# Performance work log

Measured on AMD Instinct MI355X. Metric: run time of the kernel, lower is better.

The kernel has to match this reference:

```python
import jax, jax.numpy as jnp
import numpy as np

D_MODEL, D_HEAD, D_MLP, N_HEADS = 768, 64, 3072, 12
BATCH, SEQ = 1, 4096
LN_EPS = 1e-05
IGNORE = -100000.0


def setup_inputs() -> dict:
    key = jax.random.key(0)
    ks = jax.random.split(key, 8)
    s = 0.02
    return {
        "resid_pre": jax.random.normal(ks[0], (BATCH, SEQ, D_MODEL), jnp.float32),
        "ln1_w": jnp.ones((D_MODEL,), jnp.float32),
        "ln1_b": jnp.zeros((D_MODEL,), jnp.float32),
        "ln2_w": jnp.ones((D_MODEL,), jnp.float32),
        "ln2_b": jnp.zeros((D_MODEL,), jnp.float32),
        "W_Q": jax.random.normal(ks[1], (N_HEADS, D_MODEL, D_HEAD), jnp.float32) * s,
        "W_K": jax.random.normal(ks[2], (N_HEADS, D_MODEL, D_HEAD), jnp.float32) * s,
        "W_V": jax.random.normal(ks[3], (N_HEADS, D_MODEL, D_HEAD), jnp.float32) * s,
        "W_O": jax.random.normal(ks[4], (N_HEADS, D_HEAD, D_MODEL), jnp.float32) * s,
        "b_Q": jnp.zeros((N_HEADS, D_HEAD), jnp.float32),
        "b_K": jnp.zeros((N_HEADS, D_HEAD), jnp.float32),
        "b_V": jnp.zeros((N_HEADS, D_HEAD), jnp.float32),
        "b_O": jnp.zeros((D_MODEL,), jnp.float32),
        "W_in": jax.random.normal(ks[5], (D_MODEL, D_MLP), jnp.float32) * s,
        "b_in": jnp.zeros((D_MLP,), jnp.float32),
        "W_out": jax.random.normal(ks[6], (D_MLP, D_MODEL), jnp.float32) * s,
        "b_out": jnp.zeros((D_MODEL,), jnp.float32),
    }


def _layernorm(x, w, b):
    mean = jnp.mean(x, axis=-1, keepdims=True)
    var = jnp.var(x, axis=-1, keepdims=True)  # unbiased=False
    return (x - mean) * jax.lax.rsqrt(var + LN_EPS) * w + b


def _attention(x, W_Q, W_K, W_V, W_O, b_Q, b_K, b_V, b_O):
    # x: [b, s, d_model]; W_{Q,K,V}: [h, d_model, d_head]
    q = jnp.einsum("bsm,hmd->bshd", x, W_Q) + b_Q
    k = jnp.einsum("bsm,hmd->bshd", x, W_K) + b_K
    v = jnp.einsum("bsm,hmd->bshd", x, W_V) + b_V
    scores = jnp.einsum("bqhd,bkhd->bhqk", q, k) / np.sqrt(D_HEAD).astype(np.float32)
    seq = x.shape[1]
    causal = jnp.tril(jnp.ones((seq, seq), bool))  # True where allowed
    scores = jnp.where(causal, scores, IGNORE)
    pattern = jax.nn.softmax(scores, axis=-1)
    z = jnp.einsum("bkhd,bhqk->bqhd", v, pattern)
    return jnp.einsum("bqhd,hdm->bqm", z, W_O) + b_O


def reference(resid_pre, ln1_w, ln1_b, ln2_w, ln2_b,
              W_Q, W_K, W_V, W_O, b_Q, b_K, b_V, b_O,
              W_in, b_in, W_out, b_out):
    resid_mid = _attention(_layernorm(resid_pre, ln1_w, ln1_b),
                           W_Q, W_K, W_V, W_O, b_Q, b_K, b_V, b_O) + resid_pre
    pre = jnp.einsum("bsm,mf->bsf", _layernorm(resid_mid, ln2_w, ln2_b), W_in) + b_in
    post = jax.nn.gelu(pre, approximate=False)  # torch F.gelu default = exact erf
    mlp_out = jnp.einsum("bsf,fm->bsm", post, W_out) + b_out
    resid_post = mlp_out + resid_mid
    return (resid_post, post)
```

## Files before the change

kernel.cpp:

```cpp
#include <hip/hip_runtime.h>
#include <hip/hip_bf16.h>
#include <math.h>

using bf16 = __hip_bfloat16;
using u16  = unsigned short;
using u32  = unsigned int;
using short8 = __attribute__((ext_vector_type(8))) short;
using f32x4  = __attribute__((ext_vector_type(4))) float;

#define AS1 __attribute__((address_space(1)))
#define AS3 __attribute__((address_space(3)))

__device__ __forceinline__ void gld_lds16(const void* g, void* l) {
  __builtin_amdgcn_global_load_lds((const AS1 u32*)g, (AS3 u32*)l, 16, 0, 0);
}

__device__ __forceinline__ bool probe_f32(const void* p) {
  return *(const u32*)p == 0x3F800000u;
}
__device__ __forceinline__ float ldf(const void* p, size_t i, bool f32) {
  return f32 ? ((const float*)p)[i] : __bfloat162float(((const bf16*)p)[i]);
}
__device__ __forceinline__ void stf(void* p, size_t i, float v, bool f32) {
  if (f32) ((float*)p)[i] = v;
  else     ((bf16*)p)[i] = __float2bfloat16(v);
}
__device__ __forceinline__ u32 cvt_pk_bf16(float lo, float hi) {
  u32 r;
  asm("v_cvt_pk_bf16_f32 %0, %1, %2" : "=v"(r) : "v"(lo), "v"(hi));
  return r;
}

__global__ __launch_bounds__(256) void ln_kernel(const void* __restrict__ x,
    const void* __restrict__ w, const void* __restrict__ b, bf16* __restrict__ out,
    const void* probe, int x_is_f32)
{
  const bool pf = probe_f32(probe);
  const bool xf = x_is_f32 ? true : pf;
  const int row = blockIdx.x, t = threadIdx.x;
  const size_t base = (size_t)row * 768;
  float v[3]; float s1 = 0.f, s2 = 0.f;
#pragma unroll
  for (int i = 0; i < 3; ++i) { float f = ldf(x, base + i*256 + t, xf); v[i] = f; s1 += f; s2 += f*f; }
#pragma unroll
  for (int off = 32; off >= 1; off >>= 1) { s1 += __shfl_xor(s1, off); s2 += __shfl_xor(s2, off); }
  __shared__ float a1[4], a2[4];
  if ((t & 63) == 0) { a1[t>>6] = s1; a2[t>>6] = s2; }
  __syncthreads();
  float S1 = a1[0]+a1[1]+a1[2]+a1[3];
  float S2 = a2[0]+a2[1]+a2[2]+a2[3];
  float mean = S1 * (1.f/768.f);
  float var  = S2 * (1.f/768.f) - mean*mean;
  float rs = rsqrtf(var + 1e-5f);
#pragma unroll
  for (int i = 0; i < 3; ++i) {
    int c = i*256 + t;
    out[base + c] = __float2bfloat16((v[i]-mean)*rs*ldf(w, c, pf) + ldf(b, c, pf));
  }
}

__global__ __launch_bounds__(256) void prep_all(
    const void* W_Q, const void* W_K, const void* W_V, const void* Wo,
    const void* Win, const void* Wout,
    const void* bQ, const void* bK, const void* bV, const void* bO,
    const void* bIn, const void* bOut,
    bf16* __restrict__ qkvT, bf16* __restrict__ WoT, bf16* __restrict__ WinT,
    bf16* __restrict__ WoutT, float* __restrict__ biasA,
    const void* __restrict__ xres, const void* lw, const void* lb,
    bf16* __restrict__ lnout, const void* probe)
{
  const bool pf = probe_f32(probe);
  const int bid = blockIdx.x;
  const int t = threadIdx.x;
  if (bid >= 6939) {
    const int row = bid - 6939;
    const size_t base = (size_t)row * 768;
    float v[3]; float s1 = 0.f, s2 = 0.f;
#pragma unroll
    for (int i = 0; i < 3; ++i) { float f = ldf(xres, base + i*256 + t, pf); v[i] = f; s1 += f; s2 += f*f; }
#pragma unroll
    for (int off = 32; off >= 1; off >>= 1) { s1 += __shfl_xor(s1, off); s2 += __shfl_xor(s2, off); }
    __shared__ float a1[4], a2[4];
    if ((t & 63) == 0) { a1[t>>6] = s1; a2[t>>6] = s2; }
    __syncthreads();
    float S1 = a1[0]+a1[1]+a1[2]+a1[3];
    float S2 = a2[0]+a2[1]+a2[2]+a2[3];
    float mean = S1 * (1.f/768.f);
    float var  = S2 * (1.f/768.f) - mean*mean;
    float rs = rsqrtf(var + 1e-5f);
#pragma unroll
    for (int i = 0; i < 3; ++i) {
      int c = i*256 + t;
      lnout[base + c] = __float2bfloat16((v[i]-mean)*rs*ldf(lw, c, pf) + ldf(lb, c, pf));
    }
    return;
  }
  if (bid >= 6912) {
    int i = (bid - 6912)*256 + t;
    float v;
    if (i < 2304)      v = (i < 768) ? ldf(bQ, i, pf) : (i < 1536 ? ldf(bK, i-768, pf) : ldf(bV, i-1536, pf));
    else if (i < 3072) v = ldf(bO, i-2304, pf);
    else if (i < 6144) v = ldf(bIn, i-3072, pf);
    else               v = ldf(bOut, i-6144, pf);
    biasA[i] = v;
    return;
  }
  const void* src; bf16* dst; int R, C, bx, by; size_t soff = 0;
  if (bid < 1728) {
    int mtx = bid / 576, within = bid % 576;
    int h = within / 48, tt = within % 48;
    by = tt >> 1; bx = tt & 1;
    src = (mtx == 0) ? W_Q : (mtx == 1 ? W_K : W_V);
    soff = (size_t)h * 49152;
    dst = qkvT + ((size_t)mtx*768 + h*64) * 768;
    R = 768; C = 64;
  } else if (bid < 2304) {
    int within = bid - 1728; bx = within % 24; by = within / 24;
    src = Wo; dst = WoT; R = 768; C = 768;
  } else if (bid < 4608) {
    int within = bid - 2304; bx = within % 96; by = within / 96;
    src = Win; dst = WinT; R = 768; C = 3072;
  } else {
    int within = bid - 4608; bx = within % 24; by = within / 24;
    src = Wout; dst = WoutT; R = 3072; C = 768;
  }
  __shared__ bf16 tile[32][33];
  const int bc = bx*32, br = by*32;
  const int tx = t & 31, ty = t >> 5;
#pragma unroll
  for (int i = 0; i < 32; i += 8)
    tile[ty+i][tx] = __float2bfloat16(ldf(src, soff + (size_t)(br+ty+i)*C + bc + tx, pf));
  __syncthreads();
#pragma unroll
  for (int i = 0; i < 32; i += 8)
    dst[(size_t)(bc+ty+i)*R + br + tx] = tile[tx][ty+i];
}

template<int MODE, int BM, int BN, int BK>
__global__ __launch_bounds__(256) void gemm_bt(const bf16* __restrict__ A,
    const bf16* __restrict__ BT, const float* __restrict__ bias,
    const void* __restrict__ res, void* __restrict__ Cout, bf16* __restrict__ aux,
    size_t outOff, const void* probe, int M, int N, int K,
    float* __restrict__ zf, float* __restrict__ sf)
{
  constexpr int MR = BM/32, NR = BN/32;
  constexpr int CH = BK/8;
  __shared__ bf16 Alds[BM*BK];
  __shared__ bf16 Blds[BN*BK];
  const int tid = threadIdx.x;
  const int lane = tid & 63, w = tid >> 6;
  const int l15 = lane & 15, l4 = lane >> 4;

  if (MODE == 0) {
    int bid = blockIdx.y * gridDim.x + blockIdx.x;
    float4 z4 = {0.f, 0.f, 0.f, 0.f};
    float4* zp = (float4*)zf + (size_t)bid*1024;
#pragma unroll
    for (int i = 0; i < 4; ++i) zp[i*256 + tid] = z4;
    if (tid < 16) ((float4*)sf)[bid*16 + tid] = z4;
  }

  const int brow = blockIdx.y * BM, bcol = blockIdx.x * BN;
  const int wr = (w >> 1) * (BM/2), wc = (w & 1) * (BN/2);
  const bf16* Ag = A  + (size_t)brow * K;
  const bf16* Bg = BT + (size_t)bcol * K;
  f32x4 acc[MR][NR];
#pragma unroll
  for (int i = 0; i < MR; ++i)
#pragma unroll
    for (int j = 0; j < NR; ++j) acc[i][j] = 0.f;

  for (int kt = 0; kt < K; kt += BK) {
#pragma unroll
    for (int i = 0; i < BM*CH/256; ++i) {
      int id = i*256 + tid, r = id / CH, cc = id % CH;
      int sw = (r ^ (r >> 3)) & 7;
      gld_lds16(Ag + (size_t)r*K + kt + ((cc ^ sw) * 8), (char*)Alds + id*16);
    }
#pragma unroll
    for (int i = 0; i < BN*CH/256; ++i) {
      int id = i*256 + tid, r = id / CH, cc = id % CH;
      int sw = (r ^ (r >> 3)) & 7;
      gld_lds16(Bg + (size_t)r*K + kt + ((cc ^ sw) * 8), (char*)Blds + id*16);
    }
    __syncthreads();
#pragma unroll
    for (int kk = 0; kk < BK/32; ++kk) {
      short8 a[MR], b[NR];
#pragma unroll
      for (int mi = 0; mi < MR; ++mi) {
        int row = wr + mi*16 + l15, sw = (row ^ (row >> 3)) & 7;
        a[mi] = *(const short8*)((const char*)Alds + row*(BK*2) + (((kk*4 + l4) ^ sw) << 4));
      }
#pragma unroll
      for (int ni = 0; ni < NR; ++ni) {
        int row = wc + ni*16 + l15, sw = (row ^ (row >> 3)) & 7;
        b[ni] = *(const short8*)((const char*)Blds + row*(BK*2) + (((kk*4 + l4) ^ sw) << 4));
      }
      __builtin_amdgcn_s_setprio(1);
#pragma unroll
      for (int mi = 0; mi < MR; ++mi)
#pragma unroll
        for (int ni = 0; ni < NR; ++ni)
          acc[mi][ni] = __builtin_amdgcn_mfma_f32_16x16x32_bf16(a[mi], b[ni], acc[mi][ni], 0, 0, 0);
      __builtin_amdgcn_s_setprio(0);
    }
    __syncthreads();
  }

  const bool pf = probe_f32(probe);
#pragma unroll
  for (int mi = 0; mi < MR; ++mi) {
#pragma unroll
    for (int r = 0; r < 4; ++r) {
      int row = brow + wr + mi*16 + l4*4 + r;
      size_t rowoff = (size_t)row * N;
#pragma unroll
      for (int ni = 0; ni < NR; ++ni) {
        int col = bcol + wc + ni*16 + l15;
        float v = acc[mi][ni][r] + bias[col];
        if (MODE == 1) v += ldf(res, rowoff + col, pf);
        if (MODE == 3) v += ((const float*)res)[rowoff + col];
        if (MODE == 2) v = 0.5f * v * (1.0f + erff(v * 0.70710678118654752f));
        if (MODE == 0) ((bf16*)Cout)[rowoff + col] = __float2bfloat16(v);
        else if (MODE == 1) ((float*)Cout)[rowoff + col] = v;
        else {
          stf(Cout, outOff + rowoff + col, v, pf);
          if (MODE == 2) aux[rowoff + col] = __float2bfloat16(v);
        }
      }
    }
  }
}

__global__ __launch_bounds__(256) void attn_kernel(const bf16* __restrict__ QKV,
    float* __restrict__ Zf, float* __restrict__ Sf)
{
  __shared__ bf16 Ks[2][4096];
  __shared__ bf16 VTs[2][4096];
  __shared__ bf16 Ps[4][1024];
  const int cid = 159 - blockIdx.x, h = blockIdx.y;
  int qb, c;
  if (cid < 16)      { qb = cid;                    c = 0; }
  else if (cid < 48) { qb = 16 + ((cid-16) >> 1);   c = (cid-16) & 1; }
  else if (cid < 96) { qb = 32 + (cid-48)/3;        c = (cid-48)%3; }
  else               { qb = 48 + ((cid-96) >> 2);   c = (cid-96) & 3; }
  const int t_lo = c*16, t_hi = min(c*16 + 16, qb + 1);

  const int tid = threadIdx.x, lane = tid & 63, w = tid >> 6;
  const int l15 = lane & 15, l4 = lane >> 4;
  const int q0 = qb * 64;

  short8 qf[2];
#pragma unroll
  for (int kk = 0; kk < 2; ++kk)
    qf[kk] = *(const short8*)(QKV + (size_t)(q0 + w*16 + l15)*2304 + h*64 + kk*32 + l4*8);

  int kaddr[2][4], pst[4], pld[2], vwa[8];
#pragma unroll
  for (int kk = 0; kk < 2; ++kk)
#pragma unroll
    for (int ct = 0; ct < 4; ++ct) {
      int krow = ct*16 + l15, sk = (krow ^ (krow >> 3)) & 7;
      kaddr[kk][ct] = krow*128 + (((kk*4 + l4) ^ sk) << 4);
    }
#pragma unroll
  for (int r = 0; r < 4; ++r) {
    int prow = l4*4 + r, sp = (prow ^ (prow >> 3)) & 7;
    pst[r] = prow*128 + (((l15 >> 1) ^ sp) << 4) + (l15 & 1)*8;
  }
#pragma unroll
  for (int kg = 0; kg < 2; ++kg) {
    int sp2 = (l15 ^ (l15 >> 3)) & 7;
    pld[kg] = l15*128 + (((kg*4 + l4) ^ sp2) << 4);
  }
  const int vw = tid >> 3, vd0 = (tid & 7) * 8;
  const int vk0 = (vw >> 1) + (vw & 1) * 32;
#pragma unroll
  for (int d = 0; d < 8; ++d) {
    int row = vd0 + d, srow = (row ^ (row >> 3)) & 7;
    vwa[d] = row*128 + (((vw >> 2) ^ srow) << 4) + (vw & 3)*4;
  }

  const ptrdiff_t STEP = 64*2304;
  int id0 = tid, r0 = id0 >> 3;
  int s0 = (r0 ^ (r0 >> 3)) & 7, c0 = ((id0 & 7) ^ s0) * 8;
  int id1 = 256 + tid, r1 = id1 >> 3;
  int s1 = (r1 ^ (r1 >> 3)) & 7, c1 = ((id1 & 7) ^ s1) * 8;
  const bf16* kgp0 = QKV + (size_t)(t_lo*64 + r0)*2304 + 768 + h*64 + c0;
  const bf16* kgp1 = QKV + (size_t)(t_lo*64 + r1)*2304 + 768 + h*64 + c1;
  const int ksd0 = id0*16, ksd1 = id1*16;
  const bf16* vgp0 = QKV + (size_t)(t_lo*64 + vk0)*2304 + 1536 + h*64 + vd0;
  const bf16* vgp1 = vgp0 + (size_t)16*2304;
  uint4 va, vb, ka, kb;

  ka = *(const uint4*)kgp0;  kgp0 += STEP;
  kb = *(const uint4*)kgp1;  kgp1 += STEP;
  va = *(const uint4*)vgp0;  vgp0 += STEP;
  vb = *(const uint4*)vgp1;  vgp1 += STEP;
  *(uint4*)((char*)Ks[0] + ksd0) = ka;
  *(uint4*)((char*)Ks[0] + ksd1) = kb;
  {
    const u16* pa = (const u16*)&va; const u16* pb = (const u16*)&vb;
#pragma unroll
    for (int d = 0; d < 8; ++d)
      *(u32*)((char*)VTs[0] + vwa[d]) = (u32)pa[d] | ((u32)pb[d] << 16);
  }
  __syncthreads();

  f32x4 o[4]; f32x4 osum;
#pragma unroll
  for (int dt = 0; dt < 4; ++dt) o[dt] = 0.f;
  osum = 0.f;
  short8 ones8;
#pragma unroll
  for (int j = 0; j < 8; ++j) ones8[j] = 0x3F80;

#define ABODY(CUR, NT) {                                                        \
    const int nt_ = (NT);                                                       \
    const bool pref_ = (nt_ + 1 < t_hi);                                        \
    if (pref_) {                                                                \
      ka = *(const uint4*)kgp0;  kgp0 += STEP;                                  \
      kb = *(const uint4*)kgp1;  kgp1 += STEP;                                  \
      va = *(const uint4*)vgp0;  vgp0 += STEP;                                  \
      vb = *(const uint4*)vgp1;  vgp1 += STEP;                                  \
    }                                                                           \
    f32x4 s4[4];                                                                \
    _Pragma("unroll") for (int ct = 0; ct < 4; ++ct) s4[ct] = 0.f;              \
    __builtin_amdgcn_s_setprio(1);                                              \
    _Pragma("unroll") for (int kk = 0; kk < 2; ++kk)                            \
      _Pragma("unroll") for (int ct = 0; ct < 4; ++ct) {                        \
        short8 bk = *(const short8*)((const char*)Ks[0] + kaddr[kk][ct] + (CUR)*8192); \
        s4[ct] = __builtin_amdgcn_mfma_f32_16x16x32_bf16(qf[kk], bk, s4[ct], 0, 0, 0); \
      }                                                                         \
    __builtin_amdgcn_s_setprio(0);                                              \
    const bool diag_ = (nt_ == qb);                                             \
    _Pragma("unroll") for (int r = 0; r < 4; ++r) {                             \
      float p_[4];                                                              \
      _Pragma("unroll") for (int ct = 0; ct < 4; ++ct) {                        \
        float sv = s4[ct][r] * 0.18033688f;                                     \
        if (diag_ && (ct*16 + l15 > w*16 + l4*4 + r)) sv = -30000.0f;           \
        p_[ct] = exp2f(fminf(sv, 43.0f));                                       \
      }                                                                         \
      uint2 pk;                                                                 \
      pk.x = cvt_pk_bf16(p_[0], p_[1]);                                         \
      pk.y = cvt_pk_bf16(p_[2], p_[3]);                                         \
      *(uint2*)((char*)&Ps[w][0] + pst[r]) = pk;                                \
    }                                                                           \
    __builtin_amdgcn_s_setprio(1);                                              \
    _Pragma("unroll") for (int kg = 0; kg < 2; ++kg) {                          \
      short8 ap = *(const short8*)((const char*)&Ps[w][0] + pld[kg]);           \
      _Pragma("unroll") for (int dt = 0; dt < 4; ++dt) {                        \
        short8 bv = *(const short8*)((const char*)VTs[0] + kaddr[kg][dt] + (CUR)*8192); \
        o[dt] = __builtin_amdgcn_mfma_f32_16x16x32_bf16(ap, bv, o[dt], 0, 0, 0); \
      }                                                                         \
      osum = __builtin_amdgcn_mfma_f32_16x16x32_bf16(ap, ones8, osum, 0, 0, 0); \
    }                                                                           \
    __builtin_amdgcn_s_setprio(0);                                              \
    if (pref_) {                                                                \
      *(uint4*)((char*)Ks[0] + ksd0 + ((CUR)^1)*8192) = ka;                     \
      *(uint4*)((char*)Ks[0] + ksd1 + ((CUR)^1)*8192) = kb;                     \
      const u16* pa_ = (const u16*)&va; const u16* pb_ = (const u16*)&vb;       \
      _Pragma("unroll") for (int d = 0; d < 8; ++d)                             \
        *(u32*)((char*)VTs[0] + vwa[d] + ((CUR)^1)*8192) = (u32)pa_[d] | ((u32)pb_[d] << 16); \
    }                                                                           \
    __syncthreads();                                                            \
  }

  const int n = t_hi - t_lo;
  int j2 = 0;
  for (; j2 + 2 <= n; j2 += 2) {
    ABODY(0, t_lo + j2);
    ABODY(1, t_lo + j2 + 1);
  }
  if (j2 < n) ABODY(0, t_lo + j2);
#undef ABODY

  const int qrow0 = q0 + w*16 + l4*4;
#pragma unroll
  for (int r = 0; r < 4; ++r)
    if (l15 == 0) unsafeAtomicAdd(&Sf[(size_t)h*4096 + qrow0 + r], osum[r]);
#pragma unroll
  for (int dt = 0; dt < 4; ++dt)
#pragma unroll
    for (int r = 0; r < 4; ++r)
      unsafeAtomicAdd(&Zf[(size_t)(qrow0 + r)*768 + h*64 + dt*16 + l15], o[dt][r]);
}

__global__ __launch_bounds__(256) void norm_z(const float* __restrict__ Zf,
    const float* __restrict__ Sf, bf16* __restrict__ Zb)
{
  const int row = blockIdx.x, t = threadIdx.x;
  const size_t base = (size_t)row * 768;
#pragma unroll
  for (int i = 0; i < 3; ++i) {
    int cx = i*256 + t;
    int hh = cx >> 6;
    Zb[base + cx] = __float2bfloat16(Zf[base + cx] * __builtin_amdgcn_rcpf(Sf[(size_t)hh*4096 + row]));
  }
}

extern "C" void kernel_launch(void* const* d_in, const int* in_sizes, int n_in,
                              void* d_out, int out_size, void* d_ws, size_t ws_size,
                              hipStream_t stream)
{
  (void)in_sizes; (void)n_in; (void)out_size; (void)ws_size;
  const void* resid_pre = d_in[0];
  const void* ln1_w = d_in[1];
  const void* ln1_b = d_in[2];
  const void* ln2_w = d_in[3];
  const void* ln2_b = d_in[4];
  const void* W_Q  = d_in[5];
  const void* W_K  = d_in[6];
  const void* W_V  = d_in[7];
  const void* W_O  = d_in[8];
  const void* b_Q  = d_in[9];
  const void* b_K  = d_in[10];
  const void* b_V  = d_in[11];
  const void* b_O  = d_in[12];
  const void* W_in  = d_in[13];
  const void* b_in  = d_in[14];
  const void* W_out = d_in[15];
  const void* b_out = d_in[16];
  const void* probe = ln1_w;

  char* ws = (char*)d_ws;
  bf16*  qkvT  = (bf16*)(ws + 0);
  bf16*  WoT   = (bf16*)(ws + 3538944);
  bf16*  WinT  = (bf16*)(ws + 4718592);
  bf16*  WoutT = (bf16*)(ws + 9437184);
  float* biasA = (float*)(ws + 14155776);
  bf16*  x1    = (bf16*)(ws + 14183424);
  bf16*  QKV   = (bf16*)(ws + 20474880);
  bf16*  Zb    = (bf16*)(ws + 39349248);
  float* mid   = (float*)(ws + 45640704);
  bf16*  x2    = (bf16*)(ws + 58223616);
  bf16*  postB = (bf16*)(ws + 20474880);
  float* Zf    = (float*)(ws + 45640704);
  float* Sf    = (float*)(ws + 58223616);

  prep_all<<<11035, 256, 0, stream>>>(W_Q, W_K, W_V, W_O, W_in, W_out,
      b_Q, b_K, b_V, b_O, b_in, b_out, qkvT, WoT, WinT, WoutT, biasA,
      resid_pre, ln1_w, ln1_b, x1, probe);

  gemm_bt<0,128,96,64><<<dim3(24,32), 256, 0, stream>>>(x1, qkvT, biasA, nullptr, QKV, nullptr, 0, probe, 4096, 2304, 768, Zf, Sf);
  attn_kernel<<<dim3(160,12), 256, 0, stream>>>(QKV, Zf, Sf);
  norm_z<<<4096, 256, 0, stream>>>(Zf, Sf, Zb);
  gemm_bt<1,64,64,128><<<dim3(12,64), 256, 0, stream>>>(Zb, WoT, biasA+2304, resid_pre, mid, nullptr, 0, probe, 4096, 768, 768, nullptr, nullptr);
  ln_kernel<<<4096, 256, 0, stream>>>(mid, ln2_w, ln2_b, x2, probe, 1);
  gemm_bt<2,128,128,64><<<dim3(24,32), 256, 0, stream>>>(x2, WinT, biasA+3072, nullptr, d_out, postB, 3145728, probe, 4096, 3072, 768, nullptr, nullptr);
  gemm_bt<3,64,64,128><<<dim3(12,64), 256, 0, stream>>>(postB, WoutT, biasA+6144, mid, d_out, nullptr, 0, probe, 4096, 768, 3072, nullptr, nullptr);
}
```

Baseline: 225.3 us.

## Double attention query tile to 128 rows per block for K/V reuse

Each attention block now handles 128 query rows, with each wave doing two 16-row fragments, instead of 64 rows. Every K/V tile loaded into LDS is therefore reused for twice as many queries, which halves K/V global loads and LDS staging per query. The split-K chunking is redone with 8-tile chunks and a new triangular index mapping, giving 144 blocks per head. The cost is higher register pressure, a larger P buffer in shared memory, and coarser work units that may balance less evenly across CUs.

```diff
diff --git a/kernel.cpp b/kernel.cpp
--- a/kernel.cpp
+++ b/kernel.cpp
@@ -238,25 +238,29 @@
 {
   __shared__ bf16 Ks[2][4096];
   __shared__ bf16 VTs[2][4096];
-  __shared__ bf16 Ps[4][1024];
-  const int cid = 159 - blockIdx.x, h = blockIdx.y;
-  int qb, c;
-  if (cid < 16)      { qb = cid;                    c = 0; }
-  else if (cid < 48) { qb = 16 + ((cid-16) >> 1);   c = (cid-16) & 1; }
-  else if (cid < 96) { qb = 32 + (cid-48)/3;        c = (cid-48)%3; }
-  else               { qb = 48 + ((cid-96) >> 2);   c = (cid-96) & 3; }
-  const int t_lo = c*16, t_hi = min(c*16 + 16, qb + 1);
+  __shared__ bf16 Ps[4][2048];
+  const int h = blockIdx.y;
+  int cid = 143 - blockIdx.x;
+  int g = 0;
+  while (cid >= 2*(g+1)*(g+2)) ++g;
+  int loc = cid - 2*g*(g+1);
+  const int qb = 4*g + loc/(g+1);
+  const int c  = loc % (g+1);
+  const int ntiles = 2*qb + 2;
+  const int t_lo = c*8, t_hi = min(t_lo + 8, ntiles);
 
   const int tid = threadIdx.x, lane = tid & 63, w = tid >> 6;
   const int l15 = lane & 15, l4 = lane >> 4;
-  const int q0 = qb * 64;
-
-  short8 qf[2];
-#pragma unroll
-  for (int kk = 0; kk < 2; ++kk)
-    qf[kk] = *(const short8*)(QKV + (size_t)(q0 + w*16 + l15)*2304 + h*64 + kk*32 + l4*8);
-
-  int kaddr[2][4], pst[4], pld[2], vwa[8];
+  const int q0 = qb * 128;
+
+  short8 qf[2][2];
+#pragma unroll
+  for (int f = 0; f < 2; ++f)
+#pragma unroll
+    for (int kk = 0; kk < 2; ++kk)
+      qf[f][kk] = *(const short8*)(QKV + (size_t)(q0 + w*32 + f*16 + l15)*2304 + h*64 + kk*32 + l4*8);
+
+  int kaddr[2][4], pst[2][4], pld[2][2], vwa[8];
 #pragma unroll
   for (int kk = 0; kk < 2; ++kk)
 #pragma unroll
@@ -265,14 +269,17 @@
       kaddr[kk][ct] = krow*128 + (((kk*4 + l4) ^ sk) << 4);
     }
 #pragma unroll
-  for (int r = 0; r < 4; ++r) {
-    int prow = l4*4 + r, sp = (prow ^ (prow >> 3)) & 7;
-    pst[r] = prow*128 + (((l15 >> 1) ^ sp) << 4) + (l15 & 1)*8;
-  }
-#pragma unroll
-  for (int kg = 0; kg < 2; ++kg) {
-    int sp2 = (l15 ^ (l15 >> 3)) & 7;
-    pld[kg] = l15*128 + (((kg*4 + l4) ^ sp2) << 4);
+  for (int f = 0; f < 2; ++f) {
+#pragma unroll
+    for (int r = 0; r < 4; ++r) {
+      int prow = f*16 + l4*4 + r, sp = (prow ^ (prow >> 3)) & 7;
+      pst[f][r] = prow*128 + (((l15 >> 1) ^ sp) << 4) + (l15 & 1)*8;
+    }
+#pragma unroll
+    for (int kg = 0; kg < 2; ++kg) {
+      int prow2 = f*16 + l15, sp2 = (prow2 ^ (prow2 >> 3)) & 7;
+      pld[f][kg] = prow2*128 + (((kg*4 + l4) ^ sp2) << 4);
+    }
   }
   const int vw = tid >> 3, vd0 = (tid & 7) * 8;
   const int vk0 = (vw >> 1) + (vw & 1) * 32;
@@ -308,10 +315,13 @@
   }
   __syncthreads();
 
-  f32x4 o[4]; f32x4 osum;
-#pragma unroll
-  for (int dt = 0; dt < 4; ++dt) o[dt] = 0.f;
-  osum = 0.f;
+  f32x4 o[2][4]; f32x4 osum[2];
+#pragma unroll
+  for (int f = 0; f < 2; ++f) {
+#pragma unroll
+    for (int dt = 0; dt < 4; ++dt) o[f][dt] = 0.f;
+    osum[f] = 0.f;
+  }
   short8 ones8;
 #pragma unroll
   for (int j = 0; j < 8; ++j) ones8[j] = 0x3F80;
@@ -325,36 +335,44 @@
       va = *(const uint4*)vgp0;  vgp0 += STEP;                                  \
       vb = *(const uint4*)vgp1;  vgp1 += STEP;                                  \
     }                                                                           \
-    f32x4 s4[4];                                                                \
-    _Pragma("unroll") for (int ct = 0; ct < 4; ++ct) s4[ct] = 0.f;              \
+    f32x4 s4[2][4];                                                             \
+    _Pragma("unroll") for (int f = 0; f < 2; ++f)                               \
+      _Pragma("unroll") for (int ct = 0; ct < 4; ++ct) s4[f][ct] = 0.f;         \
     __builtin_amdgcn_s_setprio(1);                                              \
     _Pragma("unroll") for (int kk = 0; kk < 2; ++kk)                            \
       _Pragma("unroll") for (int ct = 0; ct < 4; ++ct) {                        \
         short8 bk = *(const short8*)((const char*)Ks[0] + kaddr[kk][ct] + (CUR)*8192); \
-        s4[ct] = __builtin_amdgcn_mfma_f32_16x16x32_bf16(qf[kk], bk, s4[ct], 0, 0, 0); \
+        _Pragma("unroll") for (int f = 0; f < 2; ++f)                           \
+          s4[f][ct] = __builtin_amdgcn_mfma_f32_16x16x32_bf16(qf[f][kk], bk, s4[f][ct], 0, 0, 0); \
       }                                                                         \
     __builtin_amdgcn_s_setprio(0);                                              \
-    const bool diag_ = (nt_ == qb);                                             \
-    _Pragma("unroll") for (int r = 0; r < 4; ++r) {                             \
-      float p_[4];                                                              \
-      _Pragma("unroll") for (int ct = 0; ct < 4; ++ct) {                        \
-        float sv = s4[ct][r] * 0.18033688f;                                     \
-        if (diag_ && (ct*16 + l15 > w*16 + l4*4 + r)) sv = -30000.0f;           \
-        p_[ct] = exp2f(fminf(sv, 43.0f));                                       \
+    const int dtile_ = nt_ - 2*qb;                                              \
+    const bool diag_ = (dtile_ >= 0);                                           \
+    _Pragma("unroll") for (int f = 0; f < 2; ++f)                               \
+      _Pragma("unroll") for (int r = 0; r < 4; ++r) {                           \
+        const int rowoff_ = w*32 + f*16 + l4*4 + r;                             \
+        float p_[4];                                                            \
+        _Pragma("unroll") for (int ct = 0; ct < 4; ++ct) {                      \
+          float sv = s4[f][ct][r] * 0.18033688f;                                \
+          if (diag_ && (dtile_*64 + ct*16 + l15 > rowoff_)) sv = -30000.0f;     \
+          p_[ct] = exp2f(fminf(sv, 43.0f));                                     \
+        }                                                                       \
+        uint2 pk;                                                               \
+        pk.x = cvt_pk_bf16(p_[0], p_[1]);                                       \
+        pk.y = cvt_pk_bf16(p_[2], p_[3]);                                       \
+        *(uint2*)((char*)&Ps[w][0] + pst[f][r]) = pk;                           \
       }                                                                         \
-      uint2 pk;                                                                 \
-      pk.x = cvt_pk_bf16(p_[0], p_[1]);                                         \
-      pk.y = cvt_pk_bf16(p_[2], p_[3]);                                         \
-      *(uint2*)((char*)&Ps[w][0] + pst[r]) = pk;                                \
-    }                                                                           \
     __builtin_amdgcn_s_setprio(1);                                              \
     _Pragma("unroll") for (int kg = 0; kg < 2; ++kg) {                          \
-      short8 ap = *(const short8*)((const char*)&Ps[w][0] + pld[kg]);           \
+      short8 ap0 = *(const short8*)((const char*)&Ps[w][0] + pld[0][kg]);       \
+      short8 ap1 = *(const short8*)((const char*)&Ps[w][0] + pld[1][kg]);       \
       _Pragma("unroll") for (int dt = 0; dt < 4; ++dt) {                        \
         short8 bv = *(const short8*)((const char*)VTs[0] + kaddr[kg][dt] + (CUR)*8192); \
-        o[dt] = __builtin_amdgcn_mfma_f32_16x16x32_bf16(ap, bv, o[dt], 0, 0, 0); \
+        o[0][dt] = __builtin_amdgcn_mfma_f32_16x16x32_bf16(ap0, bv, o[0][dt], 0, 0, 0); \
+        o[1][dt] = __builtin_amdgcn_mfma_f32_16x16x32_bf16(ap1, bv, o[1][dt], 0, 0, 0); \
       }                                                                         \
-      osum = __builtin_amdgcn_mfma_f32_16x16x32_bf16(ap, ones8, osum, 0, 0, 0); \
+      osum[0] = __builtin_amdgcn_mfma_f32_16x16x32_bf16(ap0, ones8, osum[0], 0, 0, 0); \
+      osum[1] = __builtin_amdgcn_mfma_f32_16x16x32_bf16(ap1, ones8, osum[1], 0, 0, 0); \
     }                                                                           \
     __builtin_amdgcn_s_setprio(0);                                              \
     if (pref_) {                                                                \
@@ -376,15 +394,18 @@
   if (j2 < n) ABODY(0, t_lo + j2);
 #undef ABODY
 
-  const int qrow0 = q0 + w*16 + l4*4;
-#pragma unroll
-  for (int r = 0; r < 4; ++r)
-    if (l15 == 0) unsafeAtomicAdd(&Sf[(size_t)h*4096 + qrow0 + r], osum[r]);
-#pragma unroll
-  for (int dt = 0; dt < 4; ++dt)
+#pragma unroll
+  for (int f = 0; f < 2; ++f) {
+    const int qrow0 = q0 + w*32 + f*16 + l4*4;
 #pragma unroll
     for (int r = 0; r < 4; ++r)
-      unsafeAtomicAdd(&Zf[(size_t)(qrow0 + r)*768 + h*64 + dt*16 + l15], o[dt][r]);
+      if (l15 == 0) unsafeAtomicAdd(&Sf[(size_t)h*4096 + qrow0 + r], osum[f][r]);
+#pragma unroll
+    for (int dt = 0; dt < 4; ++dt)
+#pragma unroll
+      for (int r = 0; r < 4; ++r)
+        unsafeAtomicAdd(&Zf[(size_t)(qrow0 + r)*768 + h*64 + dt*16 + l15], o[f][dt][r]);
+  }
 }
 
 __global__ __launch_bounds__(256) void norm_z(const float* __restrict__ Zf,
@@ -444,7 +465,7 @@
       resid_pre, ln1_w, ln1_b, x1, probe);
 
   gemm_bt<0,128,96,64><<<dim3(24,32), 256, 0, stream>>>(x1, qkvT, biasA, nullptr, QKV, nullptr, 0, probe, 4096, 2304, 768, Zf, Sf);
-  attn_kernel<<<dim3(160,12), 256, 0, stream>>>(QKV, Zf, Sf);
+  attn_kernel<<<dim3(144,12), 256, 0, stream>>>(QKV, Zf, Sf);
   norm_z<<<4096, 256, 0, stream>>>(Zf, Sf, Zb);
   gemm_bt<1,64,64,128><<<dim3(12,64), 256, 0, stream>>>(Zb, WoT, biasA+2304, resid_pre, mid, nullptr, 0, probe, 4096, 768, 768, nullptr, nullptr);
   ln_kernel<<<4096, 256, 0, stream>>>(mid, ln2_w, ln2_b, x2, probe, 1);
```

New measurement: 241.0 us. +6.9%, slower.
